# Performance work log

Hardware: AMD Instinct MI355X
Metric: run time of the kernel (lower is better)

Reference implementation:

```python
import jax, jax.numpy as jnp
import numpy as np

N_NODES = 50000
N_EDGES = 800000
IN_DIM = 32
HID = 64
OUT_DIM = 4
HEADS = 4
LAYERS = 3
N_GRAPHS = 50
NEG_SLOPE = 0.2
BN_EPS = 1e-5


def setup_inputs() -> dict:
    key = jax.random.key(0)
    ks = jax.random.split(key, 20)
    x = jax.random.normal(ks[0], (N_NODES, IN_DIM), dtype=jnp.float32)
    edge_index = jax.random.randint(ks[1], (2, N_EDGES), 0, N_NODES, dtype=jnp.int64)
    batch = jnp.sort(jax.random.randint(ks[2], (N_NODES,), 0, N_GRAPHS, dtype=jnp.int64))
    s = 0.05
    inp = {
        "x": x,
        "edge_index": edge_index,
        "batch": batch,
        "in_W": jax.random.normal(ks[3], (IN_DIM, HID), jnp.float32) * s,
        "in_b": jnp.zeros((HID,), jnp.float32),
        "gat_W": jax.random.normal(ks[4], (LAYERS, HID, HEADS * HID), jnp.float32) * s,
        "att_src": jax.random.normal(ks[5], (LAYERS, HEADS, HID), jnp.float32) * s,
        "att_dst": jax.random.normal(ks[6], (LAYERS, HEADS, HID), jnp.float32) * s,
        "gat_b": jnp.zeros((LAYERS, HID), jnp.float32),
        "bn_g": jnp.ones((LAYERS, HID), jnp.float32),
        "bn_b": jnp.zeros((LAYERS, HID), jnp.float32),
        "bn_m": jnp.zeros((LAYERS, HID), jnp.float32),
        "bn_v": jnp.ones((LAYERS, HID), jnp.float32),
        "fc1_W": jax.random.normal(ks[7], (HID, HID), jnp.float32) * s,
        "fc1_b": jnp.zeros((HID,), jnp.float32),
        "fc2_W": jax.random.normal(ks[8], (HID, OUT_DIM), jnp.float32) * s,
        "fc2_b": jnp.zeros((OUT_DIM,), jnp.float32),
    }
    return inp


def _gat_layer(x, src, dst, W, a_src, a_dst, b):
    # x: [N, HID]; src/dst: [E'] (self-loops included)
    N = x.shape[0]
    xt = (x @ W).reshape(N, HEADS, HID)           # [N, H, C]
    sc_src = jnp.einsum("nhc,hc->nh", xt, a_src)  # [N, H]
    sc_dst = jnp.einsum("nhc,hc->nh", xt, a_dst)
    e = jax.nn.leaky_relu(sc_src[src] + sc_dst[dst], NEG_SLOPE)  # [E, H]
    # segment softmax over incoming edges of each dst node
    emax = jax.ops.segment_max(e, dst, num_segments=N)
    ex = jnp.exp(e - emax[dst])
    denom = jax.ops.segment_sum(ex, dst, num_segments=N)
    alpha = ex / (denom[dst] + 1e-16)             # [E, H]
    msg = xt[src] * alpha[:, :, None]             # [E, H, C]
    out = jax.ops.segment_sum(msg, dst, num_segments=N)  # [N, H, C]
    return out.mean(axis=1) + b                   # head-average (concat=False)


def reference(x, edge_index, batch, in_W, in_b, gat_W, att_src, att_dst, gat_b,
              bn_g, bn_b, bn_m, bn_v, fc1_W, fc1_b, fc2_W, fc2_b):
    N = x.shape[0]
    loops = jnp.arange(N, dtype=edge_index.dtype)
    src = jnp.concatenate([edge_index[0], loops])
    dst = jnp.concatenate([edge_index[1], loops])

    h = x @ in_W + in_b  # dropout: eval mode (identity)
    for i in range(LAYERS):
        identity = h
        h = _gat_layer(h, src, dst, gat_W[i], att_src[i], att_dst[i], gat_b[i])
        # BatchNorm1d in eval mode (running stats)
        h = (h - bn_m[i]) * jax.lax.rsqrt(bn_v[i] + BN_EPS) * bn_g[i] + bn_b[i]
        h = jax.nn.relu(h)
        h = h + identity

    # global mean pool over graphs
    sums = jax.ops.segment_sum(h, batch, num_segments=N_GRAPHS)
    cnt = jax.ops.segment_sum(jnp.ones((N,), h.dtype), batch, num_segments=N_GRAPHS)
    g = sums / jnp.maximum(cnt, 1.0)[:, None]     # [N_GRAPHS, HID]

    g = jax.nn.relu(g @ fc1_W + fc1_b)
    return g @ fc2_W + fc2_b                      # [N_GRAPHS, OUT_DIM]
```

## Files before the change

### kernel.cpp

```cpp
#include <hip/hip_runtime.h>
#include <hip/hip_fp16.h>
#include <math.h>

#define HID 64
#define HEADS 4
#define HC 256
#define IN_DIM 32
#define NEG 0.2f
#define BN_EPS 1e-5f
#define CAP 64

typedef _Float16 f16;
typedef _Float16 f16x8 __attribute__((ext_vector_type(8)));
typedef float f32x4 __attribute__((ext_vector_type(4)));

__device__ __forceinline__ int ld_idx(const int* __restrict__ p, int i, int f64) {
    return f64 ? p[(size_t)2 * i] : p[i];
}

__global__ void k_init(const int* __restrict__ ei, int* __restrict__ flag,
                       int* __restrict__ deg, float* __restrict__ gsum,
                       int N, int NG) {
    int i = blockIdx.x * blockDim.x + threadIdx.x;
    if (i == 0) {
        int z = 1;
#pragma unroll
        for (int k = 1; k < 64; k += 2) z &= (ei[k] == 0);
        *flag = z;
    }
    if (i < N) deg[i] = 0;
    if (i < NG) gsum[i] = 0.f;
}

__global__ void k_build(const int* __restrict__ ei, const int* __restrict__ flagp,
                        int* __restrict__ deg, unsigned short* __restrict__ src_pad,
                        int E) {
    int e = blockIdx.x * blockDim.x + threadIdx.x;
    if (e >= E) return;
    const int f = *flagp;
    int s = ld_idx(ei, e, f);
    int d = ld_idx(ei, E + e, f);
    int pos = atomicAdd(&deg[d], 1);
    if (pos < CAP) src_pad[(size_t)d * CAP + pos] = (unsigned short)s;
}

__global__ void k_wtilde(const float* __restrict__ gat_W, const float* __restrict__ asrc,
                         const float* __restrict__ adst, float* __restrict__ wts,
                         float* __restrict__ wtd) {
    int l = blockIdx.x;
    int t = threadIdx.x;
    int hh = t >> 6, k = t & 63;
    const float* W = gat_W + (size_t)l * HID * HC + (size_t)k * HC + hh * HID;
    const float* as = asrc + (size_t)l * HEADS * HID + hh * HID;
    const float* ad = adst + (size_t)l * HEADS * HID + hh * HID;
    float s1 = 0.f, s2 = 0.f;
#pragma unroll
    for (int c = 0; c < HID; ++c) { s1 += W[c] * as[c]; s2 += W[c] * ad[c]; }
    wts[l * HC + hh * HID + k] = s1;
    wtd[l * HC + hh * HID + k] = s2;
}

__global__ void k_prepB(const float* __restrict__ gat_W, __half* __restrict__ BT) {
    int l = blockIdx.x;
    int t = threadIdx.x;
    int c = t & 63, jg = t >> 6;
    const float* W = gat_W + (size_t)l * HID * HC;
    __half* o = BT + (size_t)l * HID * HC + (size_t)c * HC + jg * 64;
#pragma unroll
    for (int jj = 0; jj < 64; ++jj)
        o[jj] = __float2half(W[(size_t)jj * HC + jg * 64 + c]);
}

__global__ __launch_bounds__(256) void k_input(
        const float* __restrict__ x, const float* __restrict__ W,
        const float* __restrict__ b, const float* __restrict__ wts0,
        const float* __restrict__ wtd0, float* __restrict__ h,
        __half* __restrict__ h16, float* __restrict__ ssrc,
        float* __restrict__ sdst, int N) {
    int w = threadIdx.x >> 6, lane = threadIdx.x & 63;
    int n = blockIdx.x * 4 + w;
    if (n >= N) return;
    float xv = x[(size_t)n * IN_DIM + (lane & 31)];
    float acc = b[lane];
#pragma unroll
    for (int k = 0; k < IN_DIM; ++k)
        acc += __shfl(xv, k, 64) * W[k * HID + lane];
    h[(size_t)n * HID + lane] = acc;
    h16[(size_t)n * HID + lane] = __float2half(acc);
    float p0 = acc * wts0[0 * HID + lane];
    float p1 = acc * wts0[1 * HID + lane];
    float p2 = acc * wts0[2 * HID + lane];
    float p3 = acc * wts0[3 * HID + lane];
    float q0 = acc * wtd0[0 * HID + lane];
    float q1 = acc * wtd0[1 * HID + lane];
    float q2 = acc * wtd0[2 * HID + lane];
    float q3 = acc * wtd0[3 * HID + lane];
#pragma unroll
    for (int m = 32; m >= 1; m >>= 1) {
        p0 += __shfl_xor(p0, m, 64); p1 += __shfl_xor(p1, m, 64);
        p2 += __shfl_xor(p2, m, 64); p3 += __shfl_xor(p3, m, 64);
        q0 += __shfl_xor(q0, m, 64); q1 += __shfl_xor(q1, m, 64);
        q2 += __shfl_xor(q2, m, 64); q3 += __shfl_xor(q3, m, 64);
    }
    if (lane == 0) {
        *(float4*)(ssrc + (size_t)n * HEADS) = make_float4(p0, p1, p2, p3);
        *(float4*)(sdst + (size_t)n * HEADS) = make_float4(q0, q1, q2, q3);
    }
}

__global__ __launch_bounds__(256) void k_gather(
        const int* __restrict__ deg, const unsigned short* __restrict__ src_pad,
        const float* __restrict__ ssrc, const float* __restrict__ sdst,
        const __half* __restrict__ h16, __half* __restrict__ agg, int N) {
    int d = blockIdx.x * 4 + (threadIdx.x >> 6);
    if (d >= N) return;
    const int lane = threadIdx.x & 63;
    const int g = lane >> 4, l16 = lane & 15;
    const int dg = min(deg[d], CAP);
    const int se = (int)src_pad[(size_t)d * CAP + lane];
    const float4 sdd = *(const float4*)(sdst + (size_t)d * HEADS);
    float den0 = 0.f, den1 = 0.f, den2 = 0.f, den3 = 0.f;
    float a00=0.f,a01=0.f,a02=0.f,a03=0.f, a10=0.f,a11=0.f,a12=0.f,a13=0.f;
    float a20=0.f,a21=0.f,a22=0.f,a23=0.f, a30=0.f,a31=0.f,a32=0.f,a33=0.f;
    {
        float4 ssd = *(const float4*)(ssrc + (size_t)d * HEADS);
        uint2 hu = *(const uint2*)(h16 + (size_t)d * HID + l16 * 4);
        float2 f01 = __half22float2(*(__half2*)&hu.x);
        float2 f23 = __half22float2(*(__half2*)&hu.y);
        if (g == 0) {
            float v0 = ssd.x + sdd.x; v0 = v0 > 0.f ? v0 : NEG * v0;
            float v1 = ssd.y + sdd.y; v1 = v1 > 0.f ? v1 : NEG * v1;
            float v2 = ssd.z + sdd.z; v2 = v2 > 0.f ? v2 : NEG * v2;
            float v3 = ssd.w + sdd.w; v3 = v3 > 0.f ? v3 : NEG * v3;
            float e0 = __expf(v0), e1 = __expf(v1), e2 = __expf(v2), e3 = __expf(v3);
            den0 = e0; den1 = e1; den2 = e2; den3 = e3;
            a00 = e0*f01.x; a01 = e0*f01.y; a02 = e0*f23.x; a03 = e0*f23.y;
            a10 = e1*f01.x; a11 = e1*f01.y; a12 = e1*f23.x; a13 = e1*f23.y;
            a20 = e2*f01.x; a21 = e2*f01.y; a22 = e2*f23.x; a23 = e2*f23.y;
            a30 = e3*f01.x; a31 = e3*f01.y; a32 = e3*f23.x; a33 = e3*f23.y;
        }
    }
    for (int b = 0; b < dg; b += 4) {
        int idx = b + g;
        bool valid = idx < dg;
        int s = __shfl(se, idx, 64);
        s = valid ? s : d;
        float4 ss = *(const float4*)(ssrc + (size_t)s * HEADS);
        uint2 hu = *(const uint2*)(h16 + (size_t)s * HID + l16 * 4);
        float u0 = ss.x + sdd.x; u0 = u0 > 0.f ? u0 : NEG * u0;
        float u1 = ss.y + sdd.y; u1 = u1 > 0.f ? u1 : NEG * u1;
        float u2 = ss.z + sdd.z; u2 = u2 > 0.f ? u2 : NEG * u2;
        float u3 = ss.w + sdd.w; u3 = u3 > 0.f ? u3 : NEG * u3;
        float e0 = valid ? __expf(u0) : 0.f;
        float e1 = valid ? __expf(u1) : 0.f;
        float e2 = valid ? __expf(u2) : 0.f;
        float e3 = valid ? __expf(u3) : 0.f;
        float2 f01 = __half22float2(*(__half2*)&hu.x);
        float2 f23 = __half22float2(*(__half2*)&hu.y);
        den0 += e0; den1 += e1; den2 += e2; den3 += e3;
        a00 += e0*f01.x; a01 += e0*f01.y; a02 += e0*f23.x; a03 += e0*f23.y;
        a10 += e1*f01.x; a11 += e1*f01.y; a12 += e1*f23.x; a13 += e1*f23.y;
        a20 += e2*f01.x; a21 += e2*f01.y; a22 += e2*f23.x; a23 += e2*f23.y;
        a30 += e3*f01.x; a31 += e3*f01.y; a32 += e3*f23.x; a33 += e3*f23.y;
    }
#define FOLD(v) { v += __shfl_xor(v, 16, 64); v += __shfl_xor(v, 32, 64); }
    FOLD(den0) FOLD(den1) FOLD(den2) FOLD(den3)
    FOLD(a00) FOLD(a01) FOLD(a02) FOLD(a03)
    FOLD(a10) FOLD(a11) FOLD(a12) FOLD(a13)
    FOLD(a20) FOLD(a21) FOLD(a22) FOLD(a23)
    FOLD(a30) FOLD(a31) FOLD(a32) FOLD(a33)
#undef FOLD
    float iv, o0, o1, o2, o3;
    if (g == 0)      { iv = 0.25f / den0; o0 = a00; o1 = a01; o2 = a02; o3 = a03; }
    else if (g == 1) { iv = 0.25f / den1; o0 = a10; o1 = a11; o2 = a12; o3 = a13; }
    else if (g == 2) { iv = 0.25f / den2; o0 = a20; o1 = a21; o2 = a22; o3 = a23; }
    else             { iv = 0.25f / den3; o0 = a30; o1 = a31; o2 = a32; o3 = a33; }
    __half2 q01 = __floats2half2_rn(o0 * iv, o1 * iv);
    __half2 q23 = __floats2half2_rn(o2 * iv, o3 * iv);
    uint2 st;
    st.x = *(unsigned int*)&q01;
    st.y = *(unsigned int*)&q23;
    *(uint2*)(agg + ((size_t)d * HC + g * HID + l16 * 4)) = st;
}

__global__ __launch_bounds__(256) void k_postW(
        const __half* __restrict__ agg, const __half* __restrict__ BT,
        const float* __restrict__ gb, const float* __restrict__ bg,
        const float* __restrict__ bb, const float* __restrict__ bm,
        const float* __restrict__ bv, const float* __restrict__ wtsn,
        const float* __restrict__ wtdn, float* __restrict__ h,
        __half* __restrict__ h16, float* __restrict__ ssrc,
        float* __restrict__ sdst, int N) {
    __shared__ float lds[64][68];
    const int t = threadIdx.x;
    const int w = t >> 6, l = t & 63;
    const int l16 = l & 15, lk = l >> 4;
    const f16* BTf = (const f16*)BT;
    const f16* af = (const f16*)agg;
    f16x8 bf[8][4];
#pragma unroll
    for (int ks = 0; ks < 8; ++ks)
#pragma unroll
        for (int nt = 0; nt < 4; ++nt)
            bf[ks][nt] = *(const f16x8*)(BTf + (size_t)(nt * 16 + l16) * HC + ks * 32 + lk * 8);
    int row = blockIdx.x * 64 + w * 16 + l16;
    int rowc = min(row, N - 1);
    f32x4 acc[4];
#pragma unroll
    for (int nt = 0; nt < 4; ++nt) acc[nt] = (f32x4){0.f, 0.f, 0.f, 0.f};
#pragma unroll
    for (int ks = 0; ks < 8; ++ks) {
        f16x8 a = *(const f16x8*)(af + (size_t)rowc * HC + ks * 32 + lk * 8);
#pragma unroll
        for (int nt = 0; nt < 4; ++nt)
            acc[nt] = __builtin_amdgcn_mfma_f32_16x16x32_f16(a, bf[ks][nt], acc[nt], 0, 0, 0);
    }
#pragma unroll
    for (int nt = 0; nt < 4; ++nt)
#pragma unroll
        for (int r = 0; r < 4; ++r)
            lds[w * 16 + lk * 4 + r][nt * 16 + l16] = acc[nt][r];
    __syncthreads();
    {
        int j = t >> 2, q = t & 3;
        int n = blockIdx.x * 64 + j;
        if (n < N) {
            int c0 = q * 16;
            float o[16];
            float* hrow = h + (size_t)n * HID;
#pragma unroll
            for (int i4 = 0; i4 < 4; ++i4) {
                int c = c0 + i4 * 4;
                float4 sv = *(const float4*)&lds[j][c];
                float4 r4 = *(const float4*)(hrow + c);
                float4 gb4 = *(const float4*)(gb + c);
                float4 bg4 = *(const float4*)(bg + c);
                float4 bb4 = *(const float4*)(bb + c);
                float4 bm4 = *(const float4*)(bm + c);
                float4 bv4 = *(const float4*)(bv + c);
                float4 ov;
                float v;
                v = sv.x + gb4.x; v = (v - bm4.x) * rsqrtf(bv4.x + BN_EPS) * bg4.x + bb4.x;
                ov.x = fmaxf(v, 0.f) + r4.x;
                v = sv.y + gb4.y; v = (v - bm4.y) * rsqrtf(bv4.y + BN_EPS) * bg4.y + bb4.y;
                ov.y = fmaxf(v, 0.f) + r4.y;
                v = sv.z + gb4.z; v = (v - bm4.z) * rsqrtf(bv4.z + BN_EPS) * bg4.z + bb4.z;
                ov.z = fmaxf(v, 0.f) + r4.z;
                v = sv.w + gb4.w; v = (v - bm4.w) * rsqrtf(bv4.w + BN_EPS) * bg4.w + bb4.w;
                ov.w = fmaxf(v, 0.f) + r4.w;
                *(float4*)(hrow + c) = ov;
                o[i4 * 4 + 0] = ov.x; o[i4 * 4 + 1] = ov.y;
                o[i4 * 4 + 2] = ov.z; o[i4 * 4 + 3] = ov.w;
            }
            {
                __half2 hp[8];
#pragma unroll
                for (int i = 0; i < 8; ++i)
                    hp[i] = __floats2half2_rn(o[2 * i], o[2 * i + 1]);
                uint4 u0, u1;
                u0.x = *(unsigned*)&hp[0]; u0.y = *(unsigned*)&hp[1];
                u0.z = *(unsigned*)&hp[2]; u0.w = *(unsigned*)&hp[3];
                u1.x = *(unsigned*)&hp[4]; u1.y = *(unsigned*)&hp[5];
                u1.z = *(unsigned*)&hp[6]; u1.w = *(unsigned*)&hp[7];
                *(uint4*)(h16 + (size_t)n * HID + c0) = u0;
                *(uint4*)(h16 + (size_t)n * HID + c0 + 8) = u1;
            }
            if (wtsn) {
                float ps0 = 0.f, ps1 = 0.f, ps2 = 0.f, ps3 = 0.f;
                float pd0 = 0.f, pd1 = 0.f, pd2 = 0.f, pd3 = 0.f;
#pragma unroll
                for (int i = 0; i < 16; ++i) {
                    int c = c0 + i;
                    float ov = o[i];
                    ps0 += ov * wtsn[0 * HID + c]; ps1 += ov * wtsn[1 * HID + c];
                    ps2 += ov * wtsn[2 * HID + c]; ps3 += ov * wtsn[3 * HID + c];
                    pd0 += ov * wtdn[0 * HID + c]; pd1 += ov * wtdn[1 * HID + c];
                    pd2 += ov * wtdn[2 * HID + c]; pd3 += ov * wtdn[3 * HID + c];
                }
#pragma unroll
                for (int m = 2; m >= 1; m >>= 1) {
                    ps0 += __shfl_xor(ps0, m, 64); ps1 += __shfl_xor(ps1, m, 64);
                    ps2 += __shfl_xor(ps2, m, 64); ps3 += __shfl_xor(ps3, m, 64);
                    pd0 += __shfl_xor(pd0, m, 64); pd1 += __shfl_xor(pd1, m, 64);
                    pd2 += __shfl_xor(pd2, m, 64); pd3 += __shfl_xor(pd3, m, 64);
                }
                if (q == 0) {
                    *(float4*)(ssrc + (size_t)n * HEADS) = make_float4(ps0, ps1, ps2, ps3);
                    *(float4*)(sdst + (size_t)n * HEADS) = make_float4(pd0, pd1, pd2, pd3);
                }
            }
        }
    }
}

#define NPBK 64
__global__ void k_pool_sum(const float* __restrict__ h, const int* __restrict__ batch,
                           const int* __restrict__ flagp, float* __restrict__ gsum, int N) {
    const int f = *flagp;
    int c = threadIdx.x;
    int n0 = blockIdx.x * NPBK;
    int n1 = min(n0 + NPBK, N);
    if (n0 >= N) return;
    int cur = ld_idx(batch, n0, f);
    float s = 0.f;
    for (int n = n0; n < n1; ++n) {
        int g = ld_idx(batch, n, f);
        if (g != cur) {
            atomicAdd(&gsum[cur * HID + c], s);
            s = 0.f;
            cur = g;
        }
        s += h[(size_t)n * HID + c];
    }
    atomicAdd(&gsum[cur * HID + c], s);
}

__device__ __forceinline__ int lower_bound_i(const int* __restrict__ a, int n, int v, int f) {
    int lo = 0, hi = n;
    while (lo < hi) {
        int mid = (lo + hi) >> 1;
        if (ld_idx(a, mid, f) < v) lo = mid + 1; else hi = mid;
    }
    return lo;
}

__global__ void k_mlp(const float* __restrict__ gsum, const int* __restrict__ batch,
                      const int* __restrict__ flagp, int N,
                      const float* __restrict__ W1, const float* __restrict__ b1,
                      const float* __restrict__ W2, const float* __restrict__ b2,
                      float* __restrict__ out, int OUTD) {
    int gg = blockIdx.x, c = threadIdx.x;
    const int f = *flagp;
    int lo = lower_bound_i(batch, N, gg, f);
    int hi = lower_bound_i(batch, N, gg + 1, f);
    float cnt = (float)(hi - lo);
    __shared__ float gs[HID];
    __shared__ float s1[HID];
    gs[c] = gsum[gg * HID + c] / fmaxf(cnt, 1.f);
    __syncthreads();
    float acc = b1[c];
#pragma unroll
    for (int k = 0; k < HID; ++k) acc += gs[k] * W1[k * HID + c];
    s1[c] = fmaxf(acc, 0.f);
    __syncthreads();
    if (c < OUTD) {
        float o = b2[c];
#pragma unroll
        for (int k = 0; k < HID; ++k) o += s1[k] * W2[k * OUTD + c];
        out[gg * OUTD + c] = o;
    }
}

extern "C" void kernel_launch(void* const* d_in, const int* in_sizes, int n_in,
                              void* d_out, int out_size, void* d_ws, size_t ws_size,
                              hipStream_t stream) {
    const float* x       = (const float*)d_in[0];
    const int*   ei_raw  = (const int*)d_in[1];
    const int*   b_raw   = (const int*)d_in[2];
    const float* in_W    = (const float*)d_in[3];
    const float* in_b    = (const float*)d_in[4];
    const float* gat_W   = (const float*)d_in[5];
    const float* att_src = (const float*)d_in[6];
    const float* att_dst = (const float*)d_in[7];
    const float* gat_b   = (const float*)d_in[8];
    const float* bn_g    = (const float*)d_in[9];
    const float* bn_b    = (const float*)d_in[10];
    const float* bn_m    = (const float*)d_in[11];
    const float* bn_v    = (const float*)d_in[12];
    const float* fc1_W   = (const float*)d_in[13];
    const float* fc1_b   = (const float*)d_in[14];
    const float* fc2_W   = (const float*)d_in[15];
    const float* fc2_b   = (const float*)d_in[16];

    const int N = in_sizes[2];
    const int E = in_sizes[1] / 2;
    const int OUTD = 4;
    const int G = out_size / OUTD;

    float*  h    = (float*)d_ws;
    __half* h16  = (__half*)(h + (size_t)N * HID);
    __half* agg  = h16 + (size_t)N * HID;
    float*  ssrc = (float*)(agg + (size_t)N * HC);
    float*  sdst = ssrc + (size_t)N * HEADS;
    float*  wts  = sdst + (size_t)N * HEADS;
    float*  wtd  = wts + 3 * HC;
    __half* BT   = (__half*)(wtd + 3 * HC);
    float*  gsum = (float*)(BT + 3 * HID * HC);
    int*    deg  = (int*)(gsum + (size_t)G * HID);
    unsigned short* src_pad = (unsigned short*)(deg + N);
    int*    flag = (int*)(src_pad + (size_t)N * CAP);

    k_init<<<(max(N, G * HID) + 255) / 256, 256, 0, stream>>>(
        ei_raw, flag, deg, gsum, N, G * HID);
    k_build<<<(E + 255) / 256, 256, 0, stream>>>(ei_raw, flag, deg, src_pad, E);
    k_wtilde<<<3, 256, 0, stream>>>(gat_W, att_src, att_dst, wts, wtd);
    k_prepB<<<3, 256, 0, stream>>>(gat_W, BT);
    k_input<<<(N + 3) / 4, 256, 0, stream>>>(x, in_W, in_b, wts, wtd, h, h16,
                                             ssrc, sdst, N);

    for (int l = 0; l < 3; ++l) {
        k_gather<<<(N + 3) / 4, 256, 0, stream>>>(
            deg, src_pad, ssrc, sdst, h16, agg, N);
        const float* wtsn = (l < 2) ? (wts + (l + 1) * HC) : nullptr;
        const float* wtdn = (l < 2) ? (wtd + (l + 1) * HC) : nullptr;
        k_postW<<<(N + 63) / 64, 256, 0, stream>>>(
            agg, BT + (size_t)l * HID * HC,
            gat_b + (size_t)l * HID, bn_g + (size_t)l * HID, bn_b + (size_t)l * HID,
            bn_m + (size_t)l * HID, bn_v + (size_t)l * HID,
            wtsn, wtdn, h, h16, ssrc, sdst, N);
    }

    k_pool_sum<<<(N + NPBK - 1) / NPBK, HID, 0, stream>>>(h, b_raw, flag, gsum, N);
    k_mlp<<<G, HID, 0, stream>>>(gsum, b_raw, flag, N, fc1_W, fc1_b, fc2_W, fc2_b,
                                 (float*)d_out, OUTD);
}
```

Measured before the change: 337.3 us.

## Partition edge-list build by destination range and merge weight prep kernels

```diff
diff --git a/kernel.cpp b/kernel.cpp
--- a/kernel.cpp
+++ b/kernel.cpp
@@ -9,6 +9,8 @@
 #define NEG 0.2f
 #define BN_EPS 1e-5f
 #define CAP 64
+#define NRANGE 8
+#define NSLICE 96
 
 typedef _Float16 f16;
 typedef _Float16 f16x8 __attribute__((ext_vector_type(8)));
@@ -32,43 +34,51 @@
     if (i < NG) gsum[i] = 0.f;
 }
 
-__global__ void k_build(const int* __restrict__ ei, const int* __restrict__ flagp,
-                        int* __restrict__ deg, unsigned short* __restrict__ src_pad,
-                        int E) {
-    int e = blockIdx.x * blockDim.x + threadIdx.x;
-    if (e >= E) return;
+__global__ __launch_bounds__(256) void k_build_part(
+        const int* __restrict__ ei, const int* __restrict__ flagp,
+        int* __restrict__ deg, unsigned short* __restrict__ src_pad,
+        int E, int N) {
     const int f = *flagp;
-    int s = ld_idx(ei, e, f);
-    int d = ld_idx(ei, E + e, f);
-    int pos = atomicAdd(&deg[d], 1);
-    if (pos < CAP) src_pad[(size_t)d * CAP + pos] = (unsigned short)s;
-}
-
-__global__ void k_wtilde(const float* __restrict__ gat_W, const float* __restrict__ asrc,
-                         const float* __restrict__ adst, float* __restrict__ wts,
-                         float* __restrict__ wtd) {
+    const int r = blockIdx.x & (NRANGE - 1);
+    const int q = blockIdx.x >> 3;
+    const int rlo = (int)((long long)r * N / NRANGE);
+    const int rhi = (int)((long long)(r + 1) * N / NRANGE);
+    const int e0 = (int)((long long)q * E / NSLICE);
+    const int e1 = (int)((long long)(q + 1) * E / NSLICE);
+    for (int e = e0 + threadIdx.x; e < e1; e += 256) {
+        int d = ld_idx(ei, E + e, f);
+        if (d >= rlo && d < rhi) {
+            int s = ld_idx(ei, e, f);
+            int pos = atomicAdd(&deg[d], 1);
+            if (pos < CAP) src_pad[(size_t)d * CAP + pos] = (unsigned short)s;
+        }
+    }
+}
+
+__global__ void k_prep(const float* __restrict__ gat_W, const float* __restrict__ asrc,
+                       const float* __restrict__ adst, float* __restrict__ wts,
+                       float* __restrict__ wtd, __half* __restrict__ BT) {
     int l = blockIdx.x;
     int t = threadIdx.x;
     int hh = t >> 6, k = t & 63;
-    const float* W = gat_W + (size_t)l * HID * HC + (size_t)k * HC + hh * HID;
-    const float* as = asrc + (size_t)l * HEADS * HID + hh * HID;
-    const float* ad = adst + (size_t)l * HEADS * HID + hh * HID;
-    float s1 = 0.f, s2 = 0.f;
-#pragma unroll
-    for (int c = 0; c < HID; ++c) { s1 += W[c] * as[c]; s2 += W[c] * ad[c]; }
-    wts[l * HC + hh * HID + k] = s1;
-    wtd[l * HC + hh * HID + k] = s2;
-}
-
-__global__ void k_prepB(const float* __restrict__ gat_W, __half* __restrict__ BT) {
-    int l = blockIdx.x;
-    int t = threadIdx.x;
-    int c = t & 63, jg = t >> 6;
-    const float* W = gat_W + (size_t)l * HID * HC;
-    __half* o = BT + (size_t)l * HID * HC + (size_t)c * HC + jg * 64;
-#pragma unroll
-    for (int jj = 0; jj < 64; ++jj)
-        o[jj] = __float2half(W[(size_t)jj * HC + jg * 64 + c]);
+    {
+        const float* W = gat_W + (size_t)l * HID * HC + (size_t)k * HC + hh * HID;
+        const float* as = asrc + (size_t)l * HEADS * HID + hh * HID;
+        const float* ad = adst + (size_t)l * HEADS * HID + hh * HID;
+        float s1 = 0.f, s2 = 0.f;
+#pragma unroll
+        for (int c = 0; c < HID; ++c) { s1 += W[c] * as[c]; s2 += W[c] * ad[c]; }
+        wts[l * HC + hh * HID + k] = s1;
+        wtd[l * HC + hh * HID + k] = s2;
+    }
+    {
+        int c = t & 63, jg = t >> 6;
+        const float* W = gat_W + (size_t)l * HID * HC;
+        __half* o = BT + (size_t)l * HID * HC + (size_t)c * HC + jg * 64;
+#pragma unroll
+        for (int jj = 0; jj < 64; ++jj)
+            o[jj] = __float2half(W[(size_t)jj * HC + jg * 64 + c]);
+    }
 }
 
 __global__ __launch_bounds__(256) void k_input(
@@ -392,9 +402,8 @@
 
     k_init<<<(max(N, G * HID) + 255) / 256, 256, 0, stream>>>(
         ei_raw, flag, deg, gsum, N, G * HID);
-    k_build<<<(E + 255) / 256, 256, 0, stream>>>(ei_raw, flag, deg, src_pad, E);
-    k_wtilde<<<3, 256, 0, stream>>>(gat_W, att_src, att_dst, wts, wtd);
-    k_prepB<<<3, 256, 0, stream>>>(gat_W, BT);
+    k_build_part<<<NRANGE * NSLICE, 256, 0, stream>>>(ei_raw, flag, deg, src_pad, E, N);
+    k_prep<<<3, 256, 0, stream>>>(gat_W, att_src, att_dst, wts, wtd, BT);
     k_input<<<(N + 3) / 4, 256, 0, stream>>>(x, in_W, in_b, wts, wtd, h, h16,
                                              ssrc, sdst, N);
 
```

Measured after the change: 333.0 us. About the same (-1.3%).
